# Kernel optimization log

Hardware: AMD Instinct MI355X
Metric: run time of the kernel (lower is better)

Reference implementation:

```python
import jax, jax.numpy as jnp
import numpy as np

EPS = 1e-7  # K.epsilon()
SR = 10.0


def setup_inputs() -> dict:
    key = jax.random.key(0)
    ks = jax.random.split(key, 6)
    B, T, D, U = 32, 1024, 512, 64
    x1 = jax.random.normal(ks[0], (B, T, D), jnp.float32)
    x2 = jax.random.normal(ks[1], (B, T, D), jnp.float32)
    w1 = jax.random.normal(ks[2], (D, U), jnp.float32) * (2.0 / (D + U)) ** 0.5
    w2 = jax.random.normal(ks[3], (T, U), jnp.float32) * (2.0 / (T + U)) ** 0.5
    w3 = jax.random.normal(ks[4], (T, U), jnp.float32) * (2.0 / (T + U)) ** 0.5
    we = jax.random.normal(ks[5], (U, 1), jnp.float32) * (2.0 / (U + 1)) ** 0.5
    return {"x1": x1, "x2": x2, "w1": w1, "w2": w2, "w3": w3, "we": we}


def _branch(xa, xb, w1, w2, w3, we):
    # ab = xa @ xb^T over feature axis: (B,T,T); aa = xa @ xa^T
    ab = jnp.einsum('btd,bsd->bts', xa, xb)
    aa = jnp.einsum('btd,bsd->bts', xa, xa)
    # hidden: (B,T,U) -> score (B,T,1)
    h = jnp.tanh(jnp.einsum('bts,su->btu', ab, w2)
                 + jnp.einsum('bts,su->btu', aa, w3)
                 + jnp.einsum('btd,du->btu', xa, w1))
    eij = (h @ we) * SR  # (B,T,1)
    ai = jnp.exp(eij)
    ww = ai / (jnp.sum(ai, axis=1, keepdims=True) + EPS)
    return xa * ww  # (B,T,D)


def reference(x1, x2, w1, w2, w3, we):
    ot1 = _branch(x1, x2, w1, w2, w3, we)
    ot2 = _branch(x2, x1, w1, w2, w3, we)
    return (ot1, ot2)
```

## Files before the change

### kernel.cpp

```cpp
#include <hip/hip_runtime.h>
#include <math.h>

#define B_ 32
#define T_ 1024
#define D_ 512
#define U_ 64
#define TS_ 4
#define TH_ (T_/TS_)
#define TC_ 32
#define TT_ 64
#define SR_ 10.0f
#define EPS_ 1e-7f

typedef __attribute__((ext_vector_type(8))) short bf16x8;
typedef __attribute__((ext_vector_type(4))) float f32x4;

#define LSTRIDE 40

__device__ __forceinline__ uint pack_hi2(float e, float o) {
    return (__float_as_uint(e) >> 16) | (__float_as_uint(o) & 0xffff0000u);
}
__device__ __forceinline__ float hi_part(float v) {
    return __uint_as_float(__float_as_uint(v) & 0xffff0000u);
}

__global__ __launch_bounds__(256, 3) void k1_partials(
    const float* __restrict__ x1, const float* __restrict__ x2,
    const float* __restrict__ w2, const float* __restrict__ w3,
    float* __restrict__ P)
{
    __shared__ ushort lds[8][64*LSTRIDE];

    const int dt  = blockIdx.x;
    const int ts  = blockIdx.y;
    const int b   = blockIdx.z;
    const int d0  = dt * 64;
    const int tid = threadIdx.x;
    const int lane = tid & 63;
    const int wid  = tid >> 6;
    const int wd   = wid & 1;
    const int wu   = wid >> 1;
    const int lr   = lane & 15;
    const int lg   = lane >> 4;
    const int col  = tid & 63;
    const int tq   = tid >> 6;

    f32x4 acc1[2][2], acc2[2][2];
    const f32x4 z = {0.f, 0.f, 0.f, 0.f};
    #pragma unroll
    for (int mi = 0; mi < 2; ++mi)
        #pragma unroll
        for (int ni = 0; ni < 2; ++ni) { acc1[mi][ni] = z; acc2[mi][ni] = z; }

    const size_t xb = (size_t)b * T_ * D_;

    for (int c = 0; c < TH_/TC_; ++c) {
        const int tb = ts*TH_ + c*TC_ + 8*tq;
        const float* ga[4] = { x1 + xb + (size_t)tb*D_ + d0 + col,
                               x2 + xb + (size_t)tb*D_ + d0 + col,
                               w2 + (size_t)tb*U_ + col,
                               w3 + (size_t)tb*U_ + col };
        const int stra[4] = { D_, D_, U_, U_ };
        #pragma unroll
        for (int a = 0; a < 4; ++a) {
            float v[8];
            #pragma unroll
            for (int j = 0; j < 8; ++j) v[j] = ga[a][(size_t)j * stra[a]];
            uint* hb = (uint*)lds[a*2];
            uint* lb = (uint*)lds[a*2+1];
            #pragma unroll
            for (int p = 0; p < 4; ++p) {
                float e = v[2*p], o = v[2*p+1];
                uint he = __float_as_uint(e) & 0xffff0000u;
                uint ho = __float_as_uint(o) & 0xffff0000u;
                float le = e - __uint_as_float(he);
                float lo = o - __uint_as_float(ho);
                int idx = col*(LSTRIDE/2) + 4*tq + p;
                hb[idx] = (he >> 16) | ho;
                lb[idx] = (__float_as_uint(le) >> 16) | (__float_as_uint(lo) & 0xffff0000u);
            }
        }
        __syncthreads();
        bf16x8 A1h[2], A1l[2], A2h[2], A2l[2];
        bf16x8 B2h[2], B2l[2], B3h[2], B3l[2];
        #pragma unroll
        for (int mi = 0; mi < 2; ++mi) {
            int off = (32*wd + 16*mi + lr)*LSTRIDE + 8*lg;
            A1h[mi] = *(const bf16x8*)&lds[0][off];
            A1l[mi] = *(const bf16x8*)&lds[1][off];
            A2h[mi] = *(const bf16x8*)&lds[2][off];
            A2l[mi] = *(const bf16x8*)&lds[3][off];
        }
        #pragma unroll
        for (int ni = 0; ni < 2; ++ni) {
            int off = (32*wu + 16*ni + lr)*LSTRIDE + 8*lg;
            B2h[ni] = *(const bf16x8*)&lds[4][off];
            B2l[ni] = *(const bf16x8*)&lds[5][off];
            B3h[ni] = *(const bf16x8*)&lds[6][off];
            B3l[ni] = *(const bf16x8*)&lds[7][off];
        }
        #pragma unroll
        for (int mi = 0; mi < 2; ++mi)
            #pragma unroll
            for (int ni = 0; ni < 2; ++ni) {
                f32x4 c1 = acc1[mi][ni];
                f32x4 c2 = acc2[mi][ni];
                c1 = __builtin_amdgcn_mfma_f32_16x16x32_bf16(A1h[mi], B3h[ni], c1, 0, 0, 0);
                c1 = __builtin_amdgcn_mfma_f32_16x16x32_bf16(A1h[mi], B3l[ni], c1, 0, 0, 0);
                c1 = __builtin_amdgcn_mfma_f32_16x16x32_bf16(A1l[mi], B3h[ni], c1, 0, 0, 0);
                c1 = __builtin_amdgcn_mfma_f32_16x16x32_bf16(A2h[mi], B2h[ni], c1, 0, 0, 0);
                c1 = __builtin_amdgcn_mfma_f32_16x16x32_bf16(A2h[mi], B2l[ni], c1, 0, 0, 0);
                c1 = __builtin_amdgcn_mfma_f32_16x16x32_bf16(A2l[mi], B2h[ni], c1, 0, 0, 0);
                c2 = __builtin_amdgcn_mfma_f32_16x16x32_bf16(A1h[mi], B2h[ni], c2, 0, 0, 0);
                c2 = __builtin_amdgcn_mfma_f32_16x16x32_bf16(A1h[mi], B2l[ni], c2, 0, 0, 0);
                c2 = __builtin_amdgcn_mfma_f32_16x16x32_bf16(A1l[mi], B2h[ni], c2, 0, 0, 0);
                c2 = __builtin_amdgcn_mfma_f32_16x16x32_bf16(A2h[mi], B3h[ni], c2, 0, 0, 0);
                c2 = __builtin_amdgcn_mfma_f32_16x16x32_bf16(A2h[mi], B3l[ni], c2, 0, 0, 0);
                c2 = __builtin_amdgcn_mfma_f32_16x16x32_bf16(A2l[mi], B3h[ni], c2, 0, 0, 0);
                acc1[mi][ni] = c1;
                acc2[mi][ni] = c2;
            }
        __syncthreads();
    }

    const size_t DU = (size_t)D_ * U_;
    const size_t base0 = (((size_t)ts*B_ + b)*2)*DU;
    #pragma unroll
    for (int mi = 0; mi < 2; ++mi)
        #pragma unroll
        for (int ni = 0; ni < 2; ++ni) {
            const int d = d0 + 32*wd + 16*mi + 4*lg;
            const int u = 32*wu + 16*ni + lr;
            #pragma unroll
            for (int r = 0; r < 4; ++r) {
                P[base0 + (size_t)(d+r)*U_ + u]      = acc1[mi][ni][r];
                P[base0 + DU + (size_t)(d+r)*U_ + u] = acc2[mi][ni][r];
            }
        }
}

__global__ __launch_bounds__(256) void k1_combine(
    const float* __restrict__ P, const float* __restrict__ w1,
    float* __restrict__ M1, float* __restrict__ M2)
{
    const int n = blockIdx.x*256 + threadIdx.x;
    const int b = n >> 13;
    const int r = n & 8191;
    const size_t du = (size_t)r * 4;
    const size_t DU = (size_t)D_ * U_;
    float4 w = *(const float4*)&w1[du];
    float4 s1 = w, s2 = w;
    #pragma unroll
    for (int ts = 0; ts < TS_; ++ts) {
        const float* Pb = P + (((size_t)ts*B_ + b)*2)*DU + du;
        float4 a = *(const float4*)&Pb[0];
        float4 c = *(const float4*)&Pb[DU];
        s1.x += a.x; s1.y += a.y; s1.z += a.z; s1.w += a.w;
        s2.x += c.x; s2.y += c.y; s2.z += c.z; s2.w += c.w;
    }
    *(float4*)&M1[(size_t)b*DU + du] = s1;
    *(float4*)&M2[(size_t)b*DU + du] = s2;
}

__global__ __launch_bounds__(256, 4) void k2_eij(
    const float* __restrict__ x1, const float* __restrict__ x2,
    const float* __restrict__ M1, const float* __restrict__ M2,
    const float* __restrict__ we, float* __restrict__ eij)
{
    __shared__ ushort xh[64*64];
    __shared__ ushort xl[64*64];
    __shared__ ushort mh[64*64];
    __shared__ ushort ml[64*64];

    const int tt = blockIdx.x;
    const int b  = blockIdx.y;
    const int br = blockIdx.z;
    const float* x = br ? x2 : x1;
    const float* M = (br ? M2 : M1) + (size_t)b * D_ * U_;
    const int tid  = threadIdx.x;
    const int lane = tid & 63;
    const int wid  = tid >> 6;
    const int lr   = lane & 15;
    const int lg   = lane >> 4;

    const int s_tl = tid >> 4;
    const int s_f4 = tid & 15;
    const int m_u  = tid & 63;
    const int m_dq = tid >> 6;

    f32x4 acc[4];
    const f32x4 z = {0.f, 0.f, 0.f, 0.f};
    #pragma unroll
    for (int ni = 0; ni < 4; ++ni) acc[ni] = z;

    float wreg[4];
    #pragma unroll
    for (int ni = 0; ni < 4; ++ni) wreg[ni] = we[ni*16 + lr];

    const size_t xbase = ((size_t)b*T_ + (size_t)tt*64) * D_;

    for (int c = 0; c < D_/64; ++c) {
        const int d0 = c*64;
        #pragma unroll
        for (int j = 0; j < 4; ++j) {
            int t = j*16 + s_tl;
            float4 v = *(const float4*)&x[xbase + (size_t)t*D_ + d0 + s_f4*4];
            float hx = hi_part(v.x), hy = hi_part(v.y), hz = hi_part(v.z), hw = hi_part(v.w);
            uint h0 = pack_hi2(v.x, v.y), h1 = pack_hi2(v.z, v.w);
            uint l0 = pack_hi2(v.x - hx, v.y - hy);
            uint l1 = pack_hi2(v.z - hz, v.w - hw);
            int cu  = s_f4*2;
            int swz = (t & 7) << 2;
            ((uint*)xh)[t*32 + ((cu  ) ^ swz)] = h0;
            ((uint*)xh)[t*32 + ((cu+1) ^ swz)] = h1;
            ((uint*)xl)[t*32 + ((cu  ) ^ swz)] = l0;
            ((uint*)xl)[t*32 + ((cu+1) ^ swz)] = l1;
        }
        {
            int swz = (m_u & 7) << 2;
            #pragma unroll
            for (int j2 = 0; j2 < 8; ++j2) {
                float e = M[(size_t)(d0 + m_dq*16 + 2*j2    )*U_ + m_u];
                float o = M[(size_t)(d0 + m_dq*16 + 2*j2 + 1)*U_ + m_u];
                float he = hi_part(e), ho = hi_part(o);
                uint hm = pack_hi2(e, o);
                uint lm = pack_hi2(e - he, o - ho);
                int cu = m_dq*8 + j2;
                ((uint*)mh)[m_u*32 + (cu ^ swz)] = hm;
                ((uint*)ml)[m_u*32 + (cu ^ swz)] = lm;
            }
        }
        __syncthreads();
        #pragma unroll
        for (int kk = 0; kk < 2; ++kk) {
            const int ar   = wid*16 + lr;
            const int aoff = ar*64 + (((lg + 4*kk)*8) ^ ((ar & 7) << 3));
            bf16x8 Ah = *(const bf16x8*)&xh[aoff];
            bf16x8 Al = *(const bf16x8*)&xl[aoff];
            #pragma unroll
            for (int ni = 0; ni < 4; ++ni) {
                const int bu   = ni*16 + lr;
                const int boff = bu*64 + (((lg + 4*kk)*8) ^ ((bu & 7) << 3));
                bf16x8 Bh = *(const bf16x8*)&mh[boff];
                bf16x8 Bl = *(const bf16x8*)&ml[boff];
                f32x4 a = acc[ni];
                a = __builtin_amdgcn_mfma_f32_16x16x32_bf16(Ah, Bh, a, 0, 0, 0);
                a = __builtin_amdgcn_mfma_f32_16x16x32_bf16(Ah, Bl, a, 0, 0, 0);
                a = __builtin_amdgcn_mfma_f32_16x16x32_bf16(Al, Bh, a, 0, 0, 0);
                acc[ni] = a;
            }
        }
        __syncthreads();
    }

    #pragma unroll
    for (int r = 0; r < 4; ++r) {
        float s = 0.f;
        #pragma unroll
        for (int ni = 0; ni < 4; ++ni) s += tanhf(acc[ni][r]) * wreg[ni];
        s += __shfl_xor(s, 1);
        s += __shfl_xor(s, 2);
        s += __shfl_xor(s, 4);
        s += __shfl_xor(s, 8);
        if (lr == 0) {
            int t = tt*64 + wid*16 + lg*4 + r;
            eij[((size_t)br*B_ + b)*T_ + t] = SR_ * s;
        }
    }
}

__global__ __launch_bounds__(256) void k45_scale(
    const float* __restrict__ x1, const float* __restrict__ x2,
    const float* __restrict__ eij, float* __restrict__ out)
{
    __shared__ float sdata[256];
    __shared__ float wws[T_];

    const int tt = blockIdx.x;
    const int b  = blockIdx.y;
    const int br = blockIdx.z;
    const int tid = threadIdx.x;
    const float* e = eij + ((size_t)br*B_ + b) * T_;

    float v[4];
    float m = -1e30f;
    #pragma unroll
    for (int i = 0; i < 4; ++i) { v[i] = e[tid + i*256]; m = fmaxf(m, v[i]); }
    sdata[tid] = m; __syncthreads();
    for (int s = 128; s > 0; s >>= 1) {
        if (tid < s) sdata[tid] = fmaxf(sdata[tid], sdata[tid+s]);
        __syncthreads();
    }
    m = sdata[0]; __syncthreads();
    float ssum = 0.f;
    #pragma unroll
    for (int i = 0; i < 4; ++i) { v[i] = expf(v[i] - m); ssum += v[i]; }
    sdata[tid] = ssum; __syncthreads();
    for (int s = 128; s > 0; s >>= 1) {
        if (tid < s) sdata[tid] += sdata[tid+s];
        __syncthreads();
    }
    const float inv = 1.0f / (sdata[0] + EPS_ * expf(-m));
    #pragma unroll
    for (int i = 0; i < 4; ++i) wws[tid + i*256] = v[i] * inv;
    __syncthreads();

    const float* x = br ? x2 : x1;
    const size_t xb4 = ((size_t)b*T_ + (size_t)tt*64) * (D_/4);
    float* o = out + (size_t)br*B_*T_*D_;
    #pragma unroll
    for (int k = 0; k < 32; ++k) {
        int idx = k*256 + tid;
        int tl  = idx >> 7;
        float w = wws[tt*64 + tl];
        float4 xv = ((const float4*)x)[xb4 + idx];
        float4 ov = {xv.x*w, xv.y*w, xv.z*w, xv.w*w};
        ((float4*)o)[xb4 + idx] = ov;
    }
}

extern "C" void kernel_launch(void* const* d_in, const int* in_sizes, int n_in,
                              void* d_out, int out_size, void* d_ws, size_t ws_size,
                              hipStream_t stream)
{
    const float* x1 = (const float*)d_in[0];
    const float* x2 = (const float*)d_in[1];
    const float* w1 = (const float*)d_in[2];
    const float* w2 = (const float*)d_in[3];
    const float* w3 = (const float*)d_in[4];
    const float* we = (const float*)d_in[5];
    float* out = (float*)d_out;
    float* ws  = (float*)d_ws;

    float* P   = ws;
    float* M1  = P   + (size_t)TS_*B_*2*D_*U_;
    float* M2  = M1  + (size_t)B_*D_*U_;
    float* eij = M2  + (size_t)B_*D_*U_;

    k1_partials<<<dim3(8, TS_, B_), 256, 0, stream>>>(x1, x2, w2, w3, P);
    k1_combine <<<dim3((B_*D_*U_/4 + 255)/256), 256, 0, stream>>>(P, w1, M1, M2);
    k2_eij     <<<dim3(T_/TT_, B_, 2), 256, 0, stream>>>(x1, x2, M1, M2, we, eij);
    k45_scale  <<<dim3(16, B_, 2), 256, 0, stream>>>(x1, x2, eij, out);
}
```

Measured before the change: 317.4 us.

## Pre-split w2/w3 into transposed bf16 hi/lo and pack M in combine

Adds a small pre-pass kernel that splits w2 and w3 into transposed bf16 hi/lo planes, so k1_partials copies them straight into LDS with 16-byte loads and skips the split arithmetic. The x loads in k1 now use float4 reads instead of strided scalar loads. k1_combine emits M already packed as hi/lo bf16 pairs, so k2 no longer splits M, and k1's occupancy hint rises from 3 to 4 blocks. The cost is an extra kernel launch and more workspace.

```diff
diff --git a/kernel.cpp b/kernel.cpp
--- a/kernel.cpp
+++ b/kernel.cpp
@@ -13,6 +13,7 @@
 #define EPS_ 1e-7f
 
 typedef __attribute__((ext_vector_type(8))) short bf16x8;
+typedef __attribute__((ext_vector_type(8))) unsigned short u16x8;
 typedef __attribute__((ext_vector_type(4))) float f32x4;
 
 #define LSTRIDE 40
@@ -23,11 +24,57 @@
 __device__ __forceinline__ float hi_part(float v) {
     return __uint_as_float(__float_as_uint(v) & 0xffff0000u);
 }
-
-__global__ __launch_bounds__(256, 3) void k1_partials(
+__device__ __forceinline__ uint packM(float s) {
+    uint hb = __float_as_uint(s) & 0xffff0000u;
+    float l = s - __uint_as_float(hb);
+    return (hb >> 16) | (__float_as_uint(l) & 0xffff0000u);
+}
+
+__global__ __launch_bounds__(256) void k0_wsplit(
+    const float* __restrict__ w2, const float* __restrict__ w3,
+    ushort* __restrict__ wT)
+{
+    __shared__ float tA[64*65];
+    __shared__ float tB[64*65];
+    const int t0  = blockIdx.x * 64;
+    const int tid = threadIdx.x;
+    const int tl  = tid >> 2;
+    const int q   = tid & 3;
+    #pragma unroll
+    for (int k = 0; k < 4; ++k) {
+        int f4 = q*4 + k;
+        float4 a = *(const float4*)&w2[(size_t)(t0+tl)*U_ + f4*4];
+        float4 b = *(const float4*)&w3[(size_t)(t0+tl)*U_ + f4*4];
+        tA[tl*65 + f4*4+0] = a.x; tA[tl*65 + f4*4+1] = a.y;
+        tA[tl*65 + f4*4+2] = a.z; tA[tl*65 + f4*4+3] = a.w;
+        tB[tl*65 + f4*4+0] = b.x; tB[tl*65 + f4*4+1] = b.y;
+        tB[tl*65 + f4*4+2] = b.z; tB[tl*65 + f4*4+3] = b.w;
+    }
+    __syncthreads();
+    const int u   = tid >> 2;
+    const int ts4 = tid & 3;
+    #pragma unroll
+    for (int k = 0; k < 4; ++k) {
+        int tb = ts4*16 + k*4;
+        float vA[4], vB[4];
+        #pragma unroll
+        for (int i = 0; i < 4; ++i) { vA[i] = tA[(tb+i)*65 + u]; vB[i] = tB[(tb+i)*65 + u]; }
+        uint2 hA = { pack_hi2(vA[0], vA[1]), pack_hi2(vA[2], vA[3]) };
+        uint2 lA = { pack_hi2(vA[0]-hi_part(vA[0]), vA[1]-hi_part(vA[1])),
+                     pack_hi2(vA[2]-hi_part(vA[2]), vA[3]-hi_part(vA[3])) };
+        uint2 hB = { pack_hi2(vB[0], vB[1]), pack_hi2(vB[2], vB[3]) };
+        uint2 lB = { pack_hi2(vB[0]-hi_part(vB[0]), vB[1]-hi_part(vB[1])),
+                     pack_hi2(vB[2]-hi_part(vB[2]), vB[3]-hi_part(vB[3])) };
+        *(uint2*)&wT[(size_t)(0*64 + u)*1024 + t0 + tb] = hA;
+        *(uint2*)&wT[(size_t)(1*64 + u)*1024 + t0 + tb] = lA;
+        *(uint2*)&wT[(size_t)(2*64 + u)*1024 + t0 + tb] = hB;
+        *(uint2*)&wT[(size_t)(3*64 + u)*1024 + t0 + tb] = lB;
+    }
+}
+
+__global__ __launch_bounds__(256, 4) void k1_partials(
     const float* __restrict__ x1, const float* __restrict__ x2,
-    const float* __restrict__ w2, const float* __restrict__ w3,
-    float* __restrict__ P)
+    const ushort* __restrict__ wT, float* __restrict__ P)
 {
     __shared__ ushort lds[8][64*LSTRIDE];
 
@@ -42,8 +89,11 @@
     const int wu   = wid >> 1;
     const int lr   = lane & 15;
     const int lg   = lane >> 4;
-    const int col  = tid & 63;
-    const int tq   = tid >> 6;
+    const int tp   = tid >> 4;
+    const int f4   = tid & 15;
+    const int wp   = tid >> 6;
+    const int wur  = (tid & 63) >> 2;
+    const int wtq  = tid & 3;
 
     f32x4 acc1[2][2], acc2[2][2];
     const f32x4 z = {0.f, 0.f, 0.f, 0.f};
@@ -55,29 +105,31 @@
     const size_t xb = (size_t)b * T_ * D_;
 
     for (int c = 0; c < TH_/TC_; ++c) {
-        const int tb = ts*TH_ + c*TC_ + 8*tq;
-        const float* ga[4] = { x1 + xb + (size_t)tb*D_ + d0 + col,
-                               x2 + xb + (size_t)tb*D_ + d0 + col,
-                               w2 + (size_t)tb*U_ + col,
-                               w3 + (size_t)tb*U_ + col };
-        const int stra[4] = { D_, D_, U_, U_ };
-        #pragma unroll
-        for (int a = 0; a < 4; ++a) {
-            float v[8];
-            #pragma unroll
-            for (int j = 0; j < 8; ++j) v[j] = ga[a][(size_t)j * stra[a]];
+        const int tb = ts*TH_ + c*TC_;
+        #pragma unroll
+        for (int a = 0; a < 2; ++a) {
+            const float* xa = a ? x2 : x1;
+            float4 ve = *(const float4*)&xa[xb + (size_t)(tb + 2*tp    )*D_ + d0 + f4*4];
+            float4 vo = *(const float4*)&xa[xb + (size_t)(tb + 2*tp + 1)*D_ + d0 + f4*4];
             uint* hb = (uint*)lds[a*2];
             uint* lb = (uint*)lds[a*2+1];
-            #pragma unroll
-            for (int p = 0; p < 4; ++p) {
-                float e = v[2*p], o = v[2*p+1];
-                uint he = __float_as_uint(e) & 0xffff0000u;
-                uint ho = __float_as_uint(o) & 0xffff0000u;
-                float le = e - __uint_as_float(he);
-                float lo = o - __uint_as_float(ho);
-                int idx = col*(LSTRIDE/2) + 4*tq + p;
-                hb[idx] = (he >> 16) | ho;
-                lb[idx] = (__float_as_uint(le) >> 16) | (__float_as_uint(lo) & 0xffff0000u);
+            float ev[4] = {ve.x, ve.y, ve.z, ve.w};
+            float ov[4] = {vo.x, vo.y, vo.z, vo.w};
+            #pragma unroll
+            for (int k = 0; k < 4; ++k) {
+                float e = ev[k], o = ov[k];
+                int idx = (f4*4 + k)*(LSTRIDE/2) + tp;
+                hb[idx] = pack_hi2(e, o);
+                lb[idx] = pack_hi2(e - hi_part(e), o - hi_part(o));
+            }
+        }
+        {
+            const ushort* wsrc = wT + (size_t)wp*64*1024;
+            #pragma unroll
+            for (int j = 0; j < 4; ++j) {
+                int u = j*16 + wur;
+                u16x8 v = *(const u16x8*)&wsrc[(size_t)u*1024 + tb + wtq*8];
+                *(u16x8*)&lds[4+wp][u*LSTRIDE + wtq*8] = v;
             }
         }
         __syncthreads();
@@ -141,7 +193,7 @@
 
 __global__ __launch_bounds__(256) void k1_combine(
     const float* __restrict__ P, const float* __restrict__ w1,
-    float* __restrict__ M1, float* __restrict__ M2)
+    uint* __restrict__ Mhl1, uint* __restrict__ Mhl2)
 {
     const int n = blockIdx.x*256 + threadIdx.x;
     const int b = n >> 13;
@@ -158,13 +210,15 @@
         s1.x += a.x; s1.y += a.y; s1.z += a.z; s1.w += a.w;
         s2.x += c.x; s2.y += c.y; s2.z += c.z; s2.w += c.w;
     }
-    *(float4*)&M1[(size_t)b*DU + du] = s1;
-    *(float4*)&M2[(size_t)b*DU + du] = s2;
+    uint4 m1 = { packM(s1.x), packM(s1.y), packM(s1.z), packM(s1.w) };
+    uint4 m2 = { packM(s2.x), packM(s2.y), packM(s2.z), packM(s2.w) };
+    *(uint4*)&Mhl1[(size_t)b*DU + du] = m1;
+    *(uint4*)&Mhl2[(size_t)b*DU + du] = m2;
 }
 
 __global__ __launch_bounds__(256, 4) void k2_eij(
     const float* __restrict__ x1, const float* __restrict__ x2,
-    const float* __restrict__ M1, const float* __restrict__ M2,
+    const uint* __restrict__ Mhl1, const uint* __restrict__ Mhl2,
     const float* __restrict__ we, float* __restrict__ eij)
 {
     __shared__ ushort xh[64*64];
@@ -176,7 +230,7 @@
     const int b  = blockIdx.y;
     const int br = blockIdx.z;
     const float* x = br ? x2 : x1;
-    const float* M = (br ? M2 : M1) + (size_t)b * D_ * U_;
+    const uint* M  = (br ? Mhl2 : Mhl1) + (size_t)b * D_ * U_;
     const int tid  = threadIdx.x;
     const int lane = tid & 63;
     const int wid  = tid >> 6;
@@ -216,19 +270,18 @@
             ((uint*)xl)[t*32 + ((cu  ) ^ swz)] = l0;
             ((uint*)xl)[t*32 + ((cu+1) ^ swz)] = l1;
         }
-        {
-            int swz = (m_u & 7) << 2;
-            #pragma unroll
-            for (int j2 = 0; j2 < 8; ++j2) {
-                float e = M[(size_t)(d0 + m_dq*16 + 2*j2    )*U_ + m_u];
-                float o = M[(size_t)(d0 + m_dq*16 + 2*j2 + 1)*U_ + m_u];
-                float he = hi_part(e), ho = hi_part(o);
-                uint hm = pack_hi2(e, o);
-                uint lm = pack_hi2(e - he, o - ho);
-                int cu = m_dq*8 + j2;
-                ((uint*)mh)[m_u*32 + (cu ^ swz)] = hm;
-                ((uint*)ml)[m_u*32 + (cu ^ swz)] = lm;
-            }
+        #pragma unroll
+        for (int k = 0; k < 2; ++k) {
+            u16x8 hv, lv;
+            #pragma unroll
+            for (int j = 0; j < 8; ++j) {
+                uint mm = M[(size_t)(d0 + m_dq*16 + k*8 + j)*U_ + m_u];
+                hv[j] = (ushort)(mm & 0xffffu);
+                lv[j] = (ushort)(mm >> 16);
+            }
+            int slot = (m_dq*2 + k) ^ (m_u & 7);
+            *(u16x8*)&mh[m_u*64 + slot*8] = hv;
+            *(u16x8*)&ml[m_u*64 + slot*8] = lv;
         }
         __syncthreads();
         #pragma unroll
@@ -332,13 +385,15 @@
     float* out = (float*)d_out;
     float* ws  = (float*)d_ws;
 
-    float* P   = ws;
-    float* M1  = P   + (size_t)TS_*B_*2*D_*U_;
-    float* M2  = M1  + (size_t)B_*D_*U_;
-    float* eij = M2  + (size_t)B_*D_*U_;
-
-    k1_partials<<<dim3(8, TS_, B_), 256, 0, stream>>>(x1, x2, w2, w3, P);
-    k1_combine <<<dim3((B_*D_*U_/4 + 255)/256), 256, 0, stream>>>(P, w1, M1, M2);
-    k2_eij     <<<dim3(T_/TT_, B_, 2), 256, 0, stream>>>(x1, x2, M1, M2, we, eij);
+    float* P    = ws;
+    uint*  Mhl1 = (uint*)(ws + (size_t)TS_*B_*2*D_*U_);
+    uint*  Mhl2 = Mhl1 + (size_t)B_*D_*U_;
+    float* eij  = (float*)(Mhl2 + (size_t)B_*D_*U_);
+    ushort* wT  = (ushort*)(eij + (size_t)2*B_*T_);
+
+    k0_wsplit  <<<dim3(16), 256, 0, stream>>>(w2, w3, wT);
+    k1_partials<<<dim3(8, TS_, B_), 256, 0, stream>>>(x1, x2, wT, P);
+    k1_combine <<<dim3((B_*D_*U_/4 + 255)/256), 256, 0, stream>>>(P, w1, Mhl1, Mhl2);
+    k2_eij     <<<dim3(T_/TT_, B_, 2), 256, 0, stream>>>(x1, x2, Mhl1, Mhl2, we, eij);
     k45_scale  <<<dim3(16, B_, 2), 256, 0, stream>>>(x1, x2, eij, out);
 }
```

Measured after the change: 326.5 us. 2.9% more time.

## Prefetch next K-chunk into registers while MFMAs run in two kernels

Applied to the files above, without the earlier changes.

Both the partial-products kernel and the score kernel now load the next chunk of global data into registers before computing on the current LDS tile. After the MFMA work they convert the prefetched data to hi/lo bf16 and write it to LDS. This is software pipelining meant to hide global-load latency behind the matrix math. It costs extra registers per thread (32 floats in k1), which could lower occupancy under launch_bounds(256,3), and each iteration now has an extra barrier.

```diff
diff --git a/kernel.cpp b/kernel.cpp
--- a/kernel.cpp
+++ b/kernel.cpp
@@ -8,6 +8,7 @@
 #define TS_ 4
 #define TH_ (T_/TS_)
 #define TC_ 32
+#define NC_ (TH_/TC_)
 #define TT_ 64
 #define SR_ 10.0f
 #define EPS_ 1e-7f
@@ -54,33 +55,49 @@
 
     const size_t xb = (size_t)b * T_ * D_;
 
-    for (int c = 0; c < TH_/TC_; ++c) {
-        const int tb = ts*TH_ + c*TC_ + 8*tq;
+    float stg[4][8];
+
+    {
+        const int tb = ts*TH_ + 8*tq;
         const float* ga[4] = { x1 + xb + (size_t)tb*D_ + d0 + col,
                                x2 + xb + (size_t)tb*D_ + d0 + col,
                                w2 + (size_t)tb*U_ + col,
                                w3 + (size_t)tb*U_ + col };
         const int stra[4] = { D_, D_, U_, U_ };
         #pragma unroll
-        for (int a = 0; a < 4; ++a) {
-            float v[8];
-            #pragma unroll
-            for (int j = 0; j < 8; ++j) v[j] = ga[a][(size_t)j * stra[a]];
-            uint* hb = (uint*)lds[a*2];
-            uint* lb = (uint*)lds[a*2+1];
-            #pragma unroll
-            for (int p = 0; p < 4; ++p) {
-                float e = v[2*p], o = v[2*p+1];
-                uint he = __float_as_uint(e) & 0xffff0000u;
-                uint ho = __float_as_uint(o) & 0xffff0000u;
-                float le = e - __uint_as_float(he);
-                float lo = o - __uint_as_float(ho);
-                int idx = col*(LSTRIDE/2) + 4*tq + p;
-                hb[idx] = (he >> 16) | ho;
-                lb[idx] = (__float_as_uint(le) >> 16) | (__float_as_uint(lo) & 0xffff0000u);
-            }
-        }
-        __syncthreads();
+        for (int a = 0; a < 4; ++a)
+            #pragma unroll
+            for (int j = 0; j < 8; ++j) stg[a][j] = ga[a][(size_t)j * stra[a]];
+    }
+    #pragma unroll
+    for (int a = 0; a < 4; ++a) {
+        uint* hb = (uint*)lds[a*2];
+        uint* lb = (uint*)lds[a*2+1];
+        #pragma unroll
+        for (int p = 0; p < 4; ++p) {
+            float e = stg[a][2*p], o = stg[a][2*p+1];
+            uint he = __float_as_uint(e) & 0xffff0000u;
+            uint ho = __float_as_uint(o) & 0xffff0000u;
+            int idx = col*(LSTRIDE/2) + 4*tq + p;
+            hb[idx] = (he >> 16) | ho;
+            lb[idx] = pack_hi2(e - __uint_as_float(he), o - __uint_as_float(ho));
+        }
+    }
+    __syncthreads();
+
+    for (int c = 0; c < NC_; ++c) {
+        if (c+1 < NC_) {
+            const int tb = ts*TH_ + (c+1)*TC_ + 8*tq;
+            const float* ga[4] = { x1 + xb + (size_t)tb*D_ + d0 + col,
+                                   x2 + xb + (size_t)tb*D_ + d0 + col,
+                                   w2 + (size_t)tb*U_ + col,
+                                   w3 + (size_t)tb*U_ + col };
+            const int stra[4] = { D_, D_, U_, U_ };
+            #pragma unroll
+            for (int a = 0; a < 4; ++a)
+                #pragma unroll
+                for (int j = 0; j < 8; ++j) stg[a][j] = ga[a][(size_t)j * stra[a]];
+        }
         bf16x8 A1h[2], A1l[2], A2h[2], A2l[2];
         bf16x8 B2h[2], B2l[2], B3h[2], B3l[2];
         #pragma unroll
@@ -121,6 +138,23 @@
                 acc2[mi][ni] = c2;
             }
         __syncthreads();
+        if (c+1 < NC_) {
+            #pragma unroll
+            for (int a = 0; a < 4; ++a) {
+                uint* hb = (uint*)lds[a*2];
+                uint* lb = (uint*)lds[a*2+1];
+                #pragma unroll
+                for (int p = 0; p < 4; ++p) {
+                    float e = stg[a][2*p], o = stg[a][2*p+1];
+                    uint he = __float_as_uint(e) & 0xffff0000u;
+                    uint ho = __float_as_uint(o) & 0xffff0000u;
+                    int idx = col*(LSTRIDE/2) + 4*tq + p;
+                    hb[idx] = (he >> 16) | ho;
+                    lb[idx] = pack_hi2(e - __uint_as_float(he), o - __uint_as_float(ho));
+                }
+            }
+        }
+        __syncthreads();
     }
 
     const size_t DU = (size_t)D_ * U_;
@@ -199,38 +233,57 @@
 
     const size_t xbase = ((size_t)b*T_ + (size_t)tt*64) * D_;
 
+    float4 sx[4];
+    float  sm[16];
+
+    #pragma unroll
+    for (int j = 0; j < 4; ++j)
+        sx[j] = *(const float4*)&x[xbase + (size_t)(j*16 + s_tl)*D_ + s_f4*4];
+    #pragma unroll
+    for (int j2 = 0; j2 < 8; ++j2) {
+        sm[2*j2  ] = M[(size_t)(m_dq*16 + 2*j2    )*U_ + m_u];
+        sm[2*j2+1] = M[(size_t)(m_dq*16 + 2*j2 + 1)*U_ + m_u];
+    }
+    #pragma unroll
+    for (int j = 0; j < 4; ++j) {
+        int t = j*16 + s_tl;
+        float4 v = sx[j];
+        uint h0 = pack_hi2(v.x, v.y), h1 = pack_hi2(v.z, v.w);
+        uint l0 = pack_hi2(v.x - hi_part(v.x), v.y - hi_part(v.y));
+        uint l1 = pack_hi2(v.z - hi_part(v.z), v.w - hi_part(v.w));
+        int cu  = s_f4*2;
+        int swz = (t & 7) << 2;
+        ((uint*)xh)[t*32 + ((cu  ) ^ swz)] = h0;
+        ((uint*)xh)[t*32 + ((cu+1) ^ swz)] = h1;
+        ((uint*)xl)[t*32 + ((cu  ) ^ swz)] = l0;
+        ((uint*)xl)[t*32 + ((cu+1) ^ swz)] = l1;
+    }
+    {
+        int swz = (m_u & 7) << 2;
+        #pragma unroll
+        for (int j2 = 0; j2 < 8; ++j2) {
+            float e = sm[2*j2], o = sm[2*j2+1];
+            uint hm = pack_hi2(e, o);
+            uint lm = pack_hi2(e - hi_part(e), o - hi_part(o));
+            int cu = m_dq*8 + j2;
+            ((uint*)mh)[m_u*32 + (cu ^ swz)] = hm;
+            ((uint*)ml)[m_u*32 + (cu ^ swz)] = lm;
+        }
+    }
+    __syncthreads();
+
     for (int c = 0; c < D_/64; ++c) {
-        const int d0 = c*64;
-        #pragma unroll
-        for (int j = 0; j < 4; ++j) {
-            int t = j*16 + s_tl;
-            float4 v = *(const float4*)&x[xbase + (size_t)t*D_ + d0 + s_f4*4];
-            float hx = hi_part(v.x), hy = hi_part(v.y), hz = hi_part(v.z), hw = hi_part(v.w);
-            uint h0 = pack_hi2(v.x, v.y), h1 = pack_hi2(v.z, v.w);
-            uint l0 = pack_hi2(v.x - hx, v.y - hy);
-            uint l1 = pack_hi2(v.z - hz, v.w - hw);
-            int cu  = s_f4*2;
-            int swz = (t & 7) << 2;
-            ((uint*)xh)[t*32 + ((cu  ) ^ swz)] = h0;
-            ((uint*)xh)[t*32 + ((cu+1) ^ swz)] = h1;
-            ((uint*)xl)[t*32 + ((cu  ) ^ swz)] = l0;
-            ((uint*)xl)[t*32 + ((cu+1) ^ swz)] = l1;
-        }
-        {
-            int swz = (m_u & 7) << 2;
+        if (c+1 < D_/64) {
+            const int d1 = (c+1)*64;
+            #pragma unroll
+            for (int j = 0; j < 4; ++j)
+                sx[j] = *(const float4*)&x[xbase + (size_t)(j*16 + s_tl)*D_ + d1 + s_f4*4];
             #pragma unroll
             for (int j2 = 0; j2 < 8; ++j2) {
-                float e = M[(size_t)(d0 + m_dq*16 + 2*j2    )*U_ + m_u];
-                float o = M[(size_t)(d0 + m_dq*16 + 2*j2 + 1)*U_ + m_u];
-                float he = hi_part(e), ho = hi_part(o);
-                uint hm = pack_hi2(e, o);
-                uint lm = pack_hi2(e - he, o - ho);
-                int cu = m_dq*8 + j2;
-                ((uint*)mh)[m_u*32 + (cu ^ swz)] = hm;
-                ((uint*)ml)[m_u*32 + (cu ^ swz)] = lm;
-            }
-        }
-        __syncthreads();
+                sm[2*j2  ] = M[(size_t)(d1 + m_dq*16 + 2*j2    )*U_ + m_u];
+                sm[2*j2+1] = M[(size_t)(d1 + m_dq*16 + 2*j2 + 1)*U_ + m_u];
+            }
+        }
         #pragma unroll
         for (int kk = 0; kk < 2; ++kk) {
             const int ar   = wid*16 + lr;
@@ -248,6 +301,33 @@
                 a = __builtin_amdgcn_mfma_f32_16x16x32_bf16(Ah, Bl, a, 0, 0, 0);
                 a = __builtin_amdgcn_mfma_f32_16x16x32_bf16(Al, Bh, a, 0, 0, 0);
                 acc[ni] = a;
+            }
+        }
+        __syncthreads();
+        if (c+1 < D_/64) {
+            #pragma unroll
+            for (int j = 0; j < 4; ++j) {
+                int t = j*16 + s_tl;
+                float4 v = sx[j];
+                uint h0 = pack_hi2(v.x, v.y), h1 = pack_hi2(v.z, v.w);
+                uint l0 = pack_hi2(v.x - hi_part(v.x), v.y - hi_part(v.y));
+                uint l1 = pack_hi2(v.z - hi_part(v.z), v.w - hi_part(v.w));
+                int cu  = s_f4*2;
+                int swz = (t & 7) << 2;
+                ((uint*)xh)[t*32 + ((cu  ) ^ swz)] = h0;
+                ((uint*)xh)[t*32 + ((cu+1) ^ swz)] = h1;
+                ((uint*)xl)[t*32 + ((cu  ) ^ swz)] = l0;
+                ((uint*)xl)[t*32 + ((cu+1) ^ swz)] = l1;
+            }
+            int swz = (m_u & 7) << 2;
+            #pragma unroll
+            for (int j2 = 0; j2 < 8; ++j2) {
+                float e = sm[2*j2], o = sm[2*j2+1];
+                uint hm = pack_hi2(e, o);
+                uint lm = pack_hi2(e - hi_part(e), o - hi_part(o));
+                int cu = m_dq*8 + j2;
+                ((uint*)mh)[m_u*32 + (cu ^ swz)] = hm;
+                ((uint*)ml)[m_u*32 + (cu ^ swz)] = lm;
             }
         }
         __syncthreads();
```

New measurement: 318.7 us. Within noise of the previous version (+0.4%).

## Prefetch next tile into registers during MFMA in both GEMM kernels

Applied to the files above, without the earlier changes.

Both the partials kernel and the projection kernel now load the next chunk's global data into registers before running the MFMAs on the current LDS tile. After a barrier they split it into hi/lo bf16 and write it to LDS with 128-bit stores. The aim is to hide global-load latency behind the matrix math and to cut the number of LDS store instructions. The cost is more registers held across the loop and a second barrier per iteration, which may reduce occupancy under launch_bounds(256,3).

```diff
diff --git a/kernel.cpp b/kernel.cpp
--- a/kernel.cpp
+++ b/kernel.cpp
@@ -8,6 +8,7 @@
 #define TS_ 4
 #define TH_ (T_/TS_)
 #define TC_ 32
+#define NC_ (TH_/TC_)
 #define TT_ 64
 #define SR_ 10.0f
 #define EPS_ 1e-7f
@@ -22,6 +23,14 @@
 }
 __device__ __forceinline__ float hi_part(float v) {
     return __uint_as_float(__float_as_uint(v) & 0xffff0000u);
+}
+__device__ __forceinline__ void pack8(const float* v, uint4& hv, uint4& lv) {
+    hv.x = pack_hi2(v[0], v[1]); hv.y = pack_hi2(v[2], v[3]);
+    hv.z = pack_hi2(v[4], v[5]); hv.w = pack_hi2(v[6], v[7]);
+    lv.x = pack_hi2(v[0]-hi_part(v[0]), v[1]-hi_part(v[1]));
+    lv.y = pack_hi2(v[2]-hi_part(v[2]), v[3]-hi_part(v[3]));
+    lv.z = pack_hi2(v[4]-hi_part(v[4]), v[5]-hi_part(v[5]));
+    lv.w = pack_hi2(v[6]-hi_part(v[6]), v[7]-hi_part(v[7]));
 }
 
 __global__ __launch_bounds__(256, 3) void k1_partials(
@@ -53,34 +62,44 @@
         for (int ni = 0; ni < 2; ++ni) { acc1[mi][ni] = z; acc2[mi][ni] = z; }
 
     const size_t xb = (size_t)b * T_ * D_;
-
-    for (int c = 0; c < TH_/TC_; ++c) {
-        const int tb = ts*TH_ + c*TC_ + 8*tq;
+    const int widx = col*(LSTRIDE/2) + 4*tq;
+
+    float stg[4][8];
+
+    {
+        const int tb = ts*TH_ + 8*tq;
         const float* ga[4] = { x1 + xb + (size_t)tb*D_ + d0 + col,
                                x2 + xb + (size_t)tb*D_ + d0 + col,
                                w2 + (size_t)tb*U_ + col,
                                w3 + (size_t)tb*U_ + col };
         const int stra[4] = { D_, D_, U_, U_ };
         #pragma unroll
-        for (int a = 0; a < 4; ++a) {
-            float v[8];
-            #pragma unroll
-            for (int j = 0; j < 8; ++j) v[j] = ga[a][(size_t)j * stra[a]];
-            uint* hb = (uint*)lds[a*2];
-            uint* lb = (uint*)lds[a*2+1];
-            #pragma unroll
-            for (int p = 0; p < 4; ++p) {
-                float e = v[2*p], o = v[2*p+1];
-                uint he = __float_as_uint(e) & 0xffff0000u;
-                uint ho = __float_as_uint(o) & 0xffff0000u;
-                float le = e - __uint_as_float(he);
-                float lo = o - __uint_as_float(ho);
-                int idx = col*(LSTRIDE/2) + 4*tq + p;
-                hb[idx] = (he >> 16) | ho;
-                lb[idx] = (__float_as_uint(le) >> 16) | (__float_as_uint(lo) & 0xffff0000u);
-            }
-        }
-        __syncthreads();
+        for (int a = 0; a < 4; ++a)
+            #pragma unroll
+            for (int j = 0; j < 8; ++j) stg[a][j] = ga[a][(size_t)j * stra[a]];
+    }
+    #pragma unroll
+    for (int a = 0; a < 4; ++a) {
+        uint4 hv, lv;
+        pack8(stg[a], hv, lv);
+        *(uint4*)&((uint*)lds[a*2  ])[widx] = hv;
+        *(uint4*)&((uint*)lds[a*2+1])[widx] = lv;
+    }
+    __syncthreads();
+
+    for (int c = 0; c < NC_; ++c) {
+        if (c+1 < NC_) {
+            const int tb = ts*TH_ + (c+1)*TC_ + 8*tq;
+            const float* ga[4] = { x1 + xb + (size_t)tb*D_ + d0 + col,
+                                   x2 + xb + (size_t)tb*D_ + d0 + col,
+                                   w2 + (size_t)tb*U_ + col,
+                                   w3 + (size_t)tb*U_ + col };
+            const int stra[4] = { D_, D_, U_, U_ };
+            #pragma unroll
+            for (int a = 0; a < 4; ++a)
+                #pragma unroll
+                for (int j = 0; j < 8; ++j) stg[a][j] = ga[a][(size_t)j * stra[a]];
+        }
         bf16x8 A1h[2], A1l[2], A2h[2], A2l[2];
         bf16x8 B2h[2], B2l[2], B3h[2], B3l[2];
         #pragma unroll
@@ -121,6 +140,16 @@
                 acc2[mi][ni] = c2;
             }
         __syncthreads();
+        if (c+1 < NC_) {
+            #pragma unroll
+            for (int a = 0; a < 4; ++a) {
+                uint4 hv, lv;
+                pack8(stg[a], hv, lv);
+                *(uint4*)&((uint*)lds[a*2  ])[widx] = hv;
+                *(uint4*)&((uint*)lds[a*2+1])[widx] = lv;
+            }
+        }
+        __syncthreads();
     }
 
     const size_t DU = (size_t)D_ * U_;
@@ -183,8 +212,8 @@
     const int lr   = lane & 15;
     const int lg   = lane >> 4;
 
-    const int s_tl = tid >> 4;
-    const int s_f4 = tid & 15;
+    const int s_t  = tid >> 2;
+    const int s_db = tid & 3;
     const int m_u  = tid & 63;
     const int m_dq = tid >> 6;
 
@@ -198,39 +227,45 @@
     for (int ni = 0; ni < 4; ++ni) wreg[ni] = we[ni*16 + lr];
 
     const size_t xbase = ((size_t)b*T_ + (size_t)tt*64) * D_;
+    const int xswz = (s_t & 7) << 2;
+    const int mswz = (m_u & 7) << 2;
+
+    float4 sx[4];
+    float  sm[16];
+
+    #pragma unroll
+    for (int k = 0; k < 4; ++k)
+        sx[k] = *(const float4*)&x[xbase + (size_t)s_t*D_ + s_db*16 + 4*k];
+    #pragma unroll
+    for (int j2 = 0; j2 < 16; ++j2)
+        sm[j2] = M[(size_t)(m_dq*16 + j2)*U_ + m_u];
+    {
+        uint4 hv, lv;
+        pack8(&sx[0].x, hv, lv);
+        *(uint4*)&((uint*)xh)[s_t*32 + ((s_db*8    ) ^ xswz)] = hv;
+        *(uint4*)&((uint*)xl)[s_t*32 + ((s_db*8    ) ^ xswz)] = lv;
+        pack8(&sx[2].x, hv, lv);
+        *(uint4*)&((uint*)xh)[s_t*32 + ((s_db*8 + 4) ^ xswz)] = hv;
+        *(uint4*)&((uint*)xl)[s_t*32 + ((s_db*8 + 4) ^ xswz)] = lv;
+        pack8(&sm[0], hv, lv);
+        *(uint4*)&((uint*)mh)[m_u*32 + ((m_dq*8    ) ^ mswz)] = hv;
+        *(uint4*)&((uint*)ml)[m_u*32 + ((m_dq*8    ) ^ mswz)] = lv;
+        pack8(&sm[8], hv, lv);
+        *(uint4*)&((uint*)mh)[m_u*32 + ((m_dq*8 + 4) ^ mswz)] = hv;
+        *(uint4*)&((uint*)ml)[m_u*32 + ((m_dq*8 + 4) ^ mswz)] = lv;
+    }
+    __syncthreads();
 
     for (int c = 0; c < D_/64; ++c) {
-        const int d0 = c*64;
-        #pragma unroll
-        for (int j = 0; j < 4; ++j) {
-            int t = j*16 + s_tl;
-            float4 v = *(const float4*)&x[xbase + (size_t)t*D_ + d0 + s_f4*4];
-            float hx = hi_part(v.x), hy = hi_part(v.y), hz = hi_part(v.z), hw = hi_part(v.w);
-            uint h0 = pack_hi2(v.x, v.y), h1 = pack_hi2(v.z, v.w);
-            uint l0 = pack_hi2(v.x - hx, v.y - hy);
-            uint l1 = pack_hi2(v.z - hz, v.w - hw);
-            int cu  = s_f4*2;
-            int swz = (t & 7) << 2;
-            ((uint*)xh)[t*32 + ((cu  ) ^ swz)] = h0;
-            ((uint*)xh)[t*32 + ((cu+1) ^ swz)] = h1;
-            ((uint*)xl)[t*32 + ((cu  ) ^ swz)] = l0;
-            ((uint*)xl)[t*32 + ((cu+1) ^ swz)] = l1;
-        }
-        {
-            int swz = (m_u & 7) << 2;
-            #pragma unroll
-            for (int j2 = 0; j2 < 8; ++j2) {
-                float e = M[(size_t)(d0 + m_dq*16 + 2*j2    )*U_ + m_u];
-                float o = M[(size_t)(d0 + m_dq*16 + 2*j2 + 1)*U_ + m_u];
-                float he = hi_part(e), ho = hi_part(o);
-                uint hm = pack_hi2(e, o);
-                uint lm = pack_hi2(e - he, o - ho);
-                int cu = m_dq*8 + j2;
-                ((uint*)mh)[m_u*32 + (cu ^ swz)] = hm;
-                ((uint*)ml)[m_u*32 + (cu ^ swz)] = lm;
-            }
-        }
-        __syncthreads();
+        if (c+1 < D_/64) {
+            const int d1 = (c+1)*64;
+            #pragma unroll
+            for (int k = 0; k < 4; ++k)
+                sx[k] = *(const float4*)&x[xbase + (size_t)s_t*D_ + d1 + s_db*16 + 4*k];
+            #pragma unroll
+            for (int j2 = 0; j2 < 16; ++j2)
+                sm[j2] = M[(size_t)(d1 + m_dq*16 + j2)*U_ + m_u];
+        }
         #pragma unroll
         for (int kk = 0; kk < 2; ++kk) {
             const int ar   = wid*16 + lr;
@@ -251,6 +286,22 @@
             }
         }
         __syncthreads();
+        if (c+1 < D_/64) {
+            uint4 hv, lv;
+            pack8(&sx[0].x, hv, lv);
+            *(uint4*)&((uint*)xh)[s_t*32 + ((s_db*8    ) ^ xswz)] = hv;
+            *(uint4*)&((uint*)xl)[s_t*32 + ((s_db*8    ) ^ xswz)] = lv;
+            pack8(&sx[2].x, hv, lv);
+            *(uint4*)&((uint*)xh)[s_t*32 + ((s_db*8 + 4) ^ xswz)] = hv;
+            *(uint4*)&((uint*)xl)[s_t*32 + ((s_db*8 + 4) ^ xswz)] = lv;
+            pack8(&sm[0], hv, lv);
+            *(uint4*)&((uint*)mh)[m_u*32 + ((m_dq*8    ) ^ mswz)] = hv;
+            *(uint4*)&((uint*)ml)[m_u*32 + ((m_dq*8    ) ^ mswz)] = lv;
+            pack8(&sm[8], hv, lv);
+            *(uint4*)&((uint*)mh)[m_u*32 + ((m_dq*8 + 4) ^ mswz)] = hv;
+            *(uint4*)&((uint*)ml)[m_u*32 + ((m_dq*8 + 4) ^ mswz)] = lv;
+        }
+        __syncthreads();
     }
 
     #pragma unroll
```

Measured after the change: 319.5 us. No clear change (+0.7%).
